# Kernel tuning notes

Measured on AMD Instinct MI355X. Metric: run time of the kernel, lower is better.

Reference implementation:

```python
import jax, jax.numpy as jnp
import numpy as np

N_LAYER, N_HEAD, D_PARAM = 4, 8, 63
BATCH, SEQ, D_FULL = 16, 2048, D_PARAM + 1
VAR = 0.02


def setup_inputs() -> dict:
    key = jax.random.key(0)
    kz, kp = jax.random.split(key)
    Z = jax.random.normal(kz, (BATCH, SEQ, D_FULL), dtype=jnp.float32)
    allparam = VAR * jax.random.normal(kp, (N_LAYER, N_HEAD, 2, D_PARAM, D_PARAM), dtype=jnp.float32)
    return {"Z": Z, "allparam": allparam}


def _augment(P, Q, d_full):
    # P_full: P in top-left block, bottom-right corner = 1, rest zeros.
    dp = P.shape[0]
    P_full = jnp.zeros((d_full, d_full), P.dtype).at[:dp, :dp].set(P).at[dp, dp].set(1.0)
    # Q_full: Q in top-left block, rest zeros (bottom-right corner stays 0).
    Q_full = jnp.zeros((d_full, d_full), Q.dtype).at[:dp, :dp].set(Q)
    return P_full, Q_full


def _attention(P, Q, Z):
    B, N, d = Z.shape
    P_full, Q_full = _augment(P, Q, d)
    # attn[b,n,m] = Z[b,n,:] @ Q_full @ Z[b,m,:]
    attn = jnp.einsum('BNi,ij,BMj->BNM', Z, Q_full, Z)
    key = jnp.einsum('ij,BNj->BNi', P_full, Z)
    # A = eye(N) with A[N-1,N-1] = 0  => zero out last token of key before aggregation.
    key = key.at[:, N - 1, :].set(0.0)
    out = jnp.einsum('BNM,BMi->BNi', attn, key)
    return out / (N - 1)


def reference(Z, allparam):
    n_layer, n_head = allparam.shape[0], allparam.shape[1]
    for i in range(n_layer):
        Zi = Z
        residues = jnp.zeros_like(Z)
        for j in range(n_head):
            residues = residues + _attention(allparam[i, j, 0], allparam[i, j, 1], Zi)
        Z = Zi + residues
    return Z
```

## Files before the change

kernel.cpp:

```cpp
#include <hip/hip_runtime.h>

constexpr int NH = 8, DP = 63, D = 64, B = 16, S = 2048;
constexpr int TILE = 128, NTILE = 16;
constexpr float INVS = 1.0f / 2047.0f;

__device__ __forceinline__ void gram_reduce_store(const float* ZN, float4* sm4,
                                                  float* __restrict__ gp, int t) {
    const int w = t >> 6, l = t & 63, qy = l >> 3, rx = l & 7;
    float g[8][8];
#pragma unroll
    for (int a = 0; a < 8; ++a)
#pragma unroll
        for (int bb = 0; bb < 8; ++bb) g[a][bb] = 0.f;

#pragma unroll 4
    for (int mi = 0; mi < 32; ++mi) {
        const int m = 32 * w + mi;
        const int f = (m >> 3) & 15;
        const float* rowp = &ZN[m * 64];
        float4 a0 = *(const float4*)&rowp[4 * (qy ^ f)];
        float4 a1 = *(const float4*)&rowp[4 * ((qy + 8) ^ f)];
        float4 b0 = *(const float4*)&rowp[4 * (rx ^ f)];
        float4 b1 = *(const float4*)&rowp[4 * ((rx + 8) ^ f)];
        float A[8]  = {a0.x, a0.y, a0.z, a0.w, a1.x, a1.y, a1.z, a1.w};
        float Bv[8] = {b0.x, b0.y, b0.z, b0.w, b1.x, b1.y, b1.z, b1.w};
#pragma unroll
        for (int a = 0; a < 8; ++a)
#pragma unroll
            for (int bb = 0; bb < 8; ++bb) g[a][bb] += A[a] * Bv[bb];
    }
    __syncthreads();

    float* part = (float*)(sm4 + w * 1024);
#pragma unroll
    for (int a = 0; a < 8; ++a) {
        const int q = 4 * qy + (a & 3) + 32 * (a >> 2);
        *(float4*)&part[q * 64 + 4 * rx]      = make_float4(g[a][0], g[a][1], g[a][2], g[a][3]);
        *(float4*)&part[q * 64 + 32 + 4 * rx] = make_float4(g[a][4], g[a][5], g[a][6], g[a][7]);
    }
    __syncthreads();

    float4* gp4 = (float4*)gp;
#pragma unroll
    for (int k = 0; k < 4; ++k) {
        const int e4 = t + 256 * k;
        float4 s0 = sm4[e4], s1 = sm4[1024 + e4], s2 = sm4[2048 + e4], s3 = sm4[3072 + e4];
        gp4[e4] = make_float4(s0.x + s1.x + s2.x + s3.x, s0.y + s1.y + s2.y + s3.y,
                              s0.z + s1.z + s2.z + s3.z, s0.w + s1.w + s2.w + s3.w);
    }
}

__global__ __launch_bounds__(256) void kGram0(const float* __restrict__ Z,
                                              float* __restrict__ Gp) {
    __shared__ float4 sm4[5120];
    float* ZN = (float*)(sm4 + 3072);
    const int b = blockIdx.x, tile = blockIdx.y, t = threadIdx.x;
#pragma unroll
    for (int k = 0; k < 8; ++k) {
        const int row = (t >> 4) + 16 * k, c4 = t & 15;
        const int grow = tile * TILE + row;
        float4 v = *(const float4*)&Z[((size_t)b * S + grow) * D + 4 * c4];
        if (grow == S - 1) v = make_float4(0.f, 0.f, 0.f, 0.f);
        *(float4*)&ZN[row * 64 + 4 * (c4 ^ ((row >> 3) & 15))] = v;
    }
    __syncthreads();
    gram_reduce_store(ZN, sm4, Gp + ((size_t)(b * 16 + tile)) * 4096, t);
}

__global__ __launch_bounds__(256) void kRed(const float* __restrict__ Gp,
                                            float* __restrict__ G,
                                            float* __restrict__ W) {
    const int b = blockIdx.x, s = blockIdx.y, t = threadIdx.x;
    const int e = s * 256 + t;
    float sum = 0.f;
#pragma unroll 4
    for (int p = 0; p < 16; ++p) sum += Gp[((size_t)(b * 16 + p)) * 4096 + e];
    G[(size_t)b * 4096 + e] = sum;
    W[(size_t)b * 4096 + e] = ((e >> 6) == (e & 63)) ? 1.f : 0.f;
}

__global__ __launch_bounds__(128) void kW(const float* __restrict__ G,
                                          const float* __restrict__ params,
                                          float* __restrict__ W) {
    __shared__ float4 sm4[(4096 + 2048 + 4096 + 2048) / 4];
    float* Gs = (float*)sm4;
    float* Pt = Gs + 4096;
    float* Qt = Pt + 2048;
    float* T  = Qt + 4096;
    const int b = blockIdx.x, j = blockIdx.y, s = blockIdx.z, t = threadIdx.x;
    const int ty = t >> 3, tx = t & 7;
    const float* P = params + (size_t)(j * 2 + 0) * (DP * DP);
    const float* Q = params + (size_t)(j * 2 + 1) * (DP * DP);

#pragma unroll
    for (int k = 0; k < 8; ++k)
        ((float4*)Gs)[t + 128 * k] = ((const float4*)(G + (size_t)b * 4096))[t + 128 * k];
#pragma unroll
    for (int k = 0; k < 16; ++k) {
        const int r = t & 63, ii = (t >> 6) + 2 * k;
        const int i = 32 * s + ii;
        float v = 0.f;
        if (r < DP && i < DP) v = P[(size_t)i * DP + r];
        else if (r == DP && i == DP) v = 1.f;
        Pt[r * 32 + 4 * ((ii >> 2) ^ (r & 7)) + (ii & 3)] = v;
    }
#pragma unroll
    for (int k = 0; k < 32; ++k) {
        const int q = t & 63, p = (t >> 6) + 2 * k;
        const float v = (p < DP && q < DP) ? Q[(size_t)p * DP + q] : 0.f;
        Qt[q * 64 + 4 * ((p >> 2) ^ (q & 15)) + (p & 3)] = v;
    }
    __syncthreads();

    float acc[4][4] = {};
#pragma unroll 4
    for (int r = 0; r < 64; ++r) {
        float4 av = *(const float4*)&Gs[r * 64 + 4 * ty];
        float4 bv = *(const float4*)&Pt[r * 32 + 4 * (tx ^ (r & 7))];
        float A[4] = {av.x, av.y, av.z, av.w}, Bb[4] = {bv.x, bv.y, bv.z, bv.w};
#pragma unroll
        for (int a = 0; a < 4; ++a)
#pragma unroll
            for (int c = 0; c < 4; ++c) acc[a][c] += A[a] * Bb[c];
    }
#pragma unroll
    for (int a = 0; a < 4; ++a)
        *(float4*)&T[(4 * ty + a) * 32 + 4 * tx] =
            make_float4(acc[a][0], acc[a][1], acc[a][2], acc[a][3]);
    __syncthreads();

    float acc2[4][4] = {};
#pragma unroll 4
    for (int q = 0; q < 64; ++q) {
        float4 av = *(const float4*)&Qt[q * 64 + 4 * (ty ^ (q & 15))];
        float4 bv = *(const float4*)&T[q * 32 + 4 * tx];
        float A[4] = {av.x, av.y, av.z, av.w}, Bb[4] = {bv.x, bv.y, bv.z, bv.w};
#pragma unroll
        for (int a = 0; a < 4; ++a)
#pragma unroll
            for (int c = 0; c < 4; ++c) acc2[a][c] += A[a] * Bb[c];
    }
    float* Wb = W + (size_t)b * 4096;
#pragma unroll
    for (int a = 0; a < 4; ++a)
#pragma unroll
        for (int c = 0; c < 4; ++c)
            atomicAdd(&Wb[(4 * ty + a) * 64 + 32 * s + 4 * tx + c], acc2[a][c] * INVS);
}

__global__ __launch_bounds__(256) void kCA(const float* __restrict__ src,
                                           const float* __restrict__ W,
                                           float* __restrict__ out,
                                           float* __restrict__ Gp, int do_gram) {
    __shared__ float4 sm4[5120];
    float* ZT = (float*)sm4;
    float* Ws = (float*)(sm4 + 2048);
    float* ZN = (float*)(sm4 + 3072);
    const int b = blockIdx.x, tile = blockIdx.y, t = threadIdx.x;
    const int ny = t & 15, ix = t >> 4;
    const size_t zbase = ((size_t)b * S + tile * TILE) * D;

#pragma unroll
    for (int k = 0; k < 4; ++k)
        sm4[2048 + t + 256 * k] = ((const float4*)(W + (size_t)b * 4096))[t + 256 * k];
#pragma unroll
    for (int k = 0; k < 8; ++k) {
        const int row = (t >> 4) + 16 * k, c4 = t & 15;
        float4 v = *(const float4*)&src[zbase + (size_t)row * D + 4 * c4];
        float vv[4] = {v.x, v.y, v.z, v.w};
#pragma unroll
        for (int c = 0; c < 4; ++c) {
            const int p = 4 * c4 + c;
            ZT[p * 128 + 4 * ((row >> 2) ^ c4) + (row & 3)] = vv[c];
        }
    }
    __syncthreads();

    float acc[8][4] = {};
#pragma unroll 4
    for (int p = 0; p < 64; ++p) {
        const int f = p >> 2;
        const float* zp = &ZT[p * 128];
        float4 a0 = *(const float4*)&zp[4 * (ny ^ f)];
        float4 a1 = *(const float4*)&zp[4 * ((ny + 16) ^ f)];
        float4 wv = *(const float4*)&Ws[p * 64 + 4 * ix];
        float A[8] = {a0.x, a0.y, a0.z, a0.w, a1.x, a1.y, a1.z, a1.w};
        float Wv[4] = {wv.x, wv.y, wv.z, wv.w};
#pragma unroll
        for (int a = 0; a < 8; ++a)
#pragma unroll
            for (int c = 0; c < 4; ++c) acc[a][c] += A[a] * Wv[c];
    }
#pragma unroll
    for (int a = 0; a < 8; ++a) {
        const int n = 4 * ny + (a & 3) + 64 * (a >> 2);
        *(float4*)&out[zbase + (size_t)n * D + 4 * ix] =
            make_float4(acc[a][0], acc[a][1], acc[a][2], acc[a][3]);
    }
    if (!do_gram) return;

#pragma unroll
    for (int a = 0; a < 8; ++a) {
        const int n = 4 * ny + (a & 3) + 64 * (a >> 2);
        float4 vv = make_float4(acc[a][0], acc[a][1], acc[a][2], acc[a][3]);
        if (tile == NTILE - 1 && n == TILE - 1) vv = make_float4(0.f, 0.f, 0.f, 0.f);
        *(float4*)&ZN[n * 64 + 4 * (ix ^ ((n >> 3) & 15))] = vv;
    }
    __syncthreads();
    gram_reduce_store(ZN, sm4, Gp + ((size_t)(b * 16 + tile)) * 4096, t);
}

extern "C" void kernel_launch(void* const* d_in, const int* in_sizes, int n_in,
                              void* d_out, int out_size, void* d_ws, size_t ws_size,
                              hipStream_t stream) {
    const float* Z        = (const float*)d_in[0];
    const float* allparam = (const float*)d_in[1];
    float* out = (float*)d_out;

    float* Gp = (float*)d_ws;
    float* G  = Gp + (size_t)B * 16 * 4096;
    float* W  = G + (size_t)B * 4096;

    kGram0<<<dim3(B, NTILE), 256, 0, stream>>>(Z, Gp);
    for (int layer = 0; layer < 4; ++layer) {
        const float* src = (layer == 0) ? Z : (const float*)out;
        const float* params = allparam + (size_t)layer * NH * 2 * DP * DP;
        kRed<<<dim3(B, 16), 256, 0, stream>>>(Gp, G, W);
        kW<<<dim3(B, NH, 2), 128, 0, stream>>>(G, params, W);
        kCA<<<dim3(B, NTILE), 256, 0, stream>>>(src, W, out, Gp, layer < 3 ? 1 : 0);
    }
}
```

Baseline: 210.5 us.

## Fuse all layers into one persistent kernel with Gram-matrix algebraic updates

Replaces the 13 separate launches with one persistent kernel of 128 blocks that synchronise through a global atomic barrier. The Gram matrix and the per-layer transforms are propagated algebraically (G' = W^T G W, M accumulated as a product of W matrices), so Z is streamed only twice, once for the initial Gram and once for the final Z·M. Launch overhead and the per-layer full passes over Z are removed. In exchange it relies on all 128 blocks being co-resident for the spin barrier, runs serialized 64x64 matmuls on only 16 blocks, and may change numerical accumulation order.

```diff
diff --git a/kernel.cpp b/kernel.cpp
--- a/kernel.cpp
+++ b/kernel.cpp
@@ -1,213 +1,312 @@
 #include <hip/hip_runtime.h>
 
-constexpr int NH = 8, DP = 63, D = 64, B = 16, S = 2048;
-constexpr int TILE = 128, NTILE = 16;
+constexpr int NH = 8, DP = 63, D = 64, BATCH = 16, S = 2048;
 constexpr float INVS = 1.0f / 2047.0f;
-
-__device__ __forceinline__ void gram_reduce_store(const float* ZN, float4* sm4,
-                                                  float* __restrict__ gp, int t) {
-    const int w = t >> 6, l = t & 63, qy = l >> 3, rx = l & 7;
-    float g[8][8];
-#pragma unroll
-    for (int a = 0; a < 8; ++a)
-#pragma unroll
-        for (int bb = 0; bb < 8; ++bb) g[a][bb] = 0.f;
-
-#pragma unroll 4
-    for (int mi = 0; mi < 32; ++mi) {
-        const int m = 32 * w + mi;
-        const int f = (m >> 3) & 15;
-        const float* rowp = &ZN[m * 64];
-        float4 a0 = *(const float4*)&rowp[4 * (qy ^ f)];
-        float4 a1 = *(const float4*)&rowp[4 * ((qy + 8) ^ f)];
-        float4 b0 = *(const float4*)&rowp[4 * (rx ^ f)];
-        float4 b1 = *(const float4*)&rowp[4 * ((rx + 8) ^ f)];
-        float A[8]  = {a0.x, a0.y, a0.z, a0.w, a1.x, a1.y, a1.z, a1.w};
-        float Bv[8] = {b0.x, b0.y, b0.z, b0.w, b1.x, b1.y, b1.z, b1.w};
-#pragma unroll
-        for (int a = 0; a < 8; ++a)
-#pragma unroll
-            for (int bb = 0; bb < 8; ++bb) g[a][bb] += A[a] * Bv[bb];
+constexpr int NBLK = 128;
+
+__device__ __forceinline__ void gsync(unsigned int* bar, unsigned int target) {
+    __syncthreads();
+    if (threadIdx.x == 0) {
+        __hip_atomic_fetch_add(bar, 1u, __ATOMIC_RELEASE, __HIP_MEMORY_SCOPE_AGENT);
+        while (__hip_atomic_load(bar, __ATOMIC_ACQUIRE, __HIP_MEMORY_SCOPE_AGENT) < target)
+            __builtin_amdgcn_s_sleep(2);
     }
     __syncthreads();
-
-    float* part = (float*)(sm4 + w * 1024);
-#pragma unroll
-    for (int a = 0; a < 8; ++a) {
-        const int q = 4 * qy + (a & 3) + 32 * (a >> 2);
-        *(float4*)&part[q * 64 + 4 * rx]      = make_float4(g[a][0], g[a][1], g[a][2], g[a][3]);
-        *(float4*)&part[q * 64 + 32 + 4 * rx] = make_float4(g[a][4], g[a][5], g[a][6], g[a][7]);
+}
+
+__global__ __launch_bounds__(256) void fused_all(
+    const float* __restrict__ Z, const float* __restrict__ params,
+    float* __restrict__ out, float* __restrict__ Gp, float* __restrict__ H,
+    float* __restrict__ Gcur, float* __restrict__ Mt, float* __restrict__ Mf,
+    unsigned int* bar) {
+    __shared__ float4 sm4[5120];
+    const int bid = blockIdx.x, t = threadIdx.x;
+    unsigned int tgt = NBLK;
+
+    {
+        float* ZN = (float*)(sm4 + 3072);
+        const int b = bid >> 3, oct = bid & 7;
+        const int w = t >> 6, l = t & 63, qy = l >> 3, rx = l & 7;
+        float g[8][8];
+#pragma unroll
+        for (int a = 0; a < 8; ++a)
+#pragma unroll
+            for (int bb = 0; bb < 8; ++bb) g[a][bb] = 0.f;
+
+        for (int half = 0; half < 2; ++half) {
+            const int rowbase = oct * 256 + half * 128;
+#pragma unroll
+            for (int k = 0; k < 8; ++k) {
+                const int row = (t >> 4) + 16 * k, c4 = t & 15;
+                const int grow = rowbase + row;
+                float4 v = *(const float4*)&Z[((size_t)b * S + grow) * D + 4 * c4];
+                if (grow == S - 1) v = make_float4(0.f, 0.f, 0.f, 0.f);
+                *(float4*)&ZN[row * 64 + 4 * (c4 ^ ((row >> 3) & 15))] = v;
+            }
+            __syncthreads();
+#pragma unroll 4
+            for (int mi = 0; mi < 32; ++mi) {
+                const int m = 32 * w + mi;
+                const int f = (m >> 3) & 15;
+                const float* rowp = &ZN[m * 64];
+                float4 a0 = *(const float4*)&rowp[4 * (qy ^ f)];
+                float4 a1 = *(const float4*)&rowp[4 * ((qy + 8) ^ f)];
+                float4 b0 = *(const float4*)&rowp[4 * (rx ^ f)];
+                float4 b1 = *(const float4*)&rowp[4 * ((rx + 8) ^ f)];
+                float A[8]  = {a0.x, a0.y, a0.z, a0.w, a1.x, a1.y, a1.z, a1.w};
+                float Bv[8] = {b0.x, b0.y, b0.z, b0.w, b1.x, b1.y, b1.z, b1.w};
+#pragma unroll
+                for (int a = 0; a < 8; ++a)
+#pragma unroll
+                    for (int bb = 0; bb < 8; ++bb) g[a][bb] += A[a] * Bv[bb];
+            }
+            __syncthreads();
+        }
+        float* part = (float*)(sm4 + w * 1024);
+#pragma unroll
+        for (int a = 0; a < 8; ++a) {
+            const int q = 4 * qy + (a & 3) + 32 * (a >> 2);
+            *(float4*)&part[q * 64 + 4 * rx]      = make_float4(g[a][0], g[a][1], g[a][2], g[a][3]);
+            *(float4*)&part[q * 64 + 32 + 4 * rx] = make_float4(g[a][4], g[a][5], g[a][6], g[a][7]);
+        }
+        __syncthreads();
+        float4* gp4 = (float4*)(Gp + (size_t)(b * 8 + oct) * 4096);
+#pragma unroll
+        for (int k = 0; k < 4; ++k) {
+            const int e4 = t + 256 * k;
+            float4 s0 = sm4[e4], s1 = sm4[1024 + e4], s2 = sm4[2048 + e4], s3 = sm4[3072 + e4];
+            gp4[e4] = make_float4(s0.x + s1.x + s2.x + s3.x, s0.y + s1.y + s2.y + s3.y,
+                                  s0.z + s1.z + s2.z + s3.z, s0.w + s1.w + s2.w + s3.w);
+        }
     }
-    __syncthreads();
-
-    float4* gp4 = (float4*)gp;
-#pragma unroll
-    for (int k = 0; k < 4; ++k) {
-        const int e4 = t + 256 * k;
-        float4 s0 = sm4[e4], s1 = sm4[1024 + e4], s2 = sm4[2048 + e4], s3 = sm4[3072 + e4];
-        gp4[e4] = make_float4(s0.x + s1.x + s2.x + s3.x, s0.y + s1.y + s2.y + s3.y,
-                              s0.z + s1.z + s2.z + s3.z, s0.w + s1.w + s2.w + s3.w);
+    gsync(bar, tgt); tgt += NBLK;
+
+    for (int layer = 0; layer < 4; ++layer) {
+        {
+            float* Gs = (float*)sm4;
+            float* Pt = Gs + 4096;
+            float* Qt = Pt + 4096;
+            float* Tb = Qt + 4096;
+            const int b = bid >> 3, j = bid & 7;
+            const float* P = params + ((size_t)(layer * NH + j) * 2) * (DP * DP);
+            const float* Q = P + DP * DP;
+            float4* Gs4 = (float4*)Gs;
+            if (layer == 0) {
+                const float4* Gp4 = (const float4*)Gp;
+#pragma unroll
+                for (int k = 0; k < 4; ++k) {
+                    const int e4 = t + 256 * k;
+                    float4 sum = make_float4(0.f, 0.f, 0.f, 0.f);
+                    for (int p = 0; p < 8; ++p) {
+                        float4 gg = Gp4[(size_t)(b * 8 + p) * 1024 + e4];
+                        sum.x += gg.x; sum.y += gg.y; sum.z += gg.z; sum.w += gg.w;
+                    }
+                    Gs4[e4] = sum;
+                }
+            } else {
+                const float4* Gc4 = (const float4*)(Gcur + (size_t)b * 4096);
+#pragma unroll
+                for (int k = 0; k < 4; ++k) Gs4[t + 256 * k] = Gc4[t + 256 * k];
+            }
+            {
+                const int rr = t & 63, qtr = t >> 6;
+#pragma unroll
+                for (int k = 0; k < 16; ++k) {
+                    const int i = qtr * 16 + k;
+                    float pv = 0.f;
+                    if (rr < DP && i < DP) pv = P[(size_t)i * DP + rr];
+                    else if (rr == DP && i == DP) pv = 1.f;
+                    Pt[rr * 64 + 4 * ((i >> 2) ^ (rr & 15)) + (i & 3)] = pv;
+                    const float qv = (i < DP && rr < DP) ? Q[(size_t)i * DP + rr] : 0.f;
+                    Qt[rr * 64 + 4 * ((i >> 2) ^ (rr & 15)) + (i & 3)] = qv;
+                }
+            }
+            __syncthreads();
+            const int ty = t >> 4, tx = t & 15;
+            float acc[4][4] = {};
+#pragma unroll 4
+            for (int r = 0; r < 64; ++r) {
+                float4 av = *(const float4*)&Gs[r * 64 + 4 * ty];
+                float4 bv = *(const float4*)&Pt[r * 64 + 4 * (tx ^ (r & 15))];
+                float A[4] = {av.x, av.y, av.z, av.w}, Bb[4] = {bv.x, bv.y, bv.z, bv.w};
+#pragma unroll
+                for (int a = 0; a < 4; ++a)
+#pragma unroll
+                    for (int c = 0; c < 4; ++c) acc[a][c] += A[a] * Bb[c];
+            }
+#pragma unroll
+            for (int a = 0; a < 4; ++a)
+                *(float4*)&Tb[(4 * ty + a) * 64 + 4 * tx] =
+                    make_float4(acc[a][0], acc[a][1], acc[a][2], acc[a][3]);
+            __syncthreads();
+            float acc2[4][4] = {};
+#pragma unroll 4
+            for (int q = 0; q < 64; ++q) {
+                float4 av = *(const float4*)&Qt[q * 64 + 4 * (ty ^ (q & 15))];
+                float4 bv = *(const float4*)&Tb[q * 64 + 4 * tx];
+                float A[4] = {av.x, av.y, av.z, av.w}, Bb[4] = {bv.x, bv.y, bv.z, bv.w};
+#pragma unroll
+                for (int a = 0; a < 4; ++a)
+#pragma unroll
+                    for (int c = 0; c < 4; ++c) acc2[a][c] += A[a] * Bb[c];
+            }
+            float* Hb = H + (size_t)(b * NH + j) * 4096;
+#pragma unroll
+            for (int a = 0; a < 4; ++a)
+                *(float4*)&Hb[(4 * ty + a) * 64 + 4 * tx] =
+                    make_float4(acc2[a][0] * INVS, acc2[a][1] * INVS,
+                                acc2[a][2] * INVS, acc2[a][3] * INVS);
+        }
+        gsync(bar, tgt); tgt += NBLK;
+
+        if (bid < 16) {
+            const int b = bid;
+            float* Ws = (float*)sm4;
+            float* As = Ws + 4096;
+            float* Ts = As + 4096;
+            float* Ms = Ts + 4096;
+            float4* Ws4 = (float4*)Ws; float4* As4 = (float4*)As; float4* Ms4 = (float4*)Ms;
+#pragma unroll
+            for (int k = 0; k < 4; ++k) {
+                const int e4 = t + 256 * k;
+                float iv[4];
+#pragma unroll
+                for (int c = 0; c < 4; ++c) {
+                    const int e = 4 * e4 + c;
+                    iv[c] = ((e >> 6) == (e & 63)) ? 1.f : 0.f;
+                }
+                float4 w = make_float4(iv[0], iv[1], iv[2], iv[3]);
+                const float4* H4 = (const float4*)H;
+                for (int j = 0; j < 8; ++j) {
+                    float4 h = H4[(size_t)(b * 8 + j) * 1024 + e4];
+                    w.x += h.x; w.y += h.y; w.z += h.z; w.w += h.w;
+                }
+                Ws4[e4] = w;
+                if (layer == 0) {
+                    const float4* Gp4 = (const float4*)Gp;
+                    float4 sum = make_float4(0.f, 0.f, 0.f, 0.f);
+                    for (int p = 0; p < 8; ++p) {
+                        float4 gg = Gp4[(size_t)(b * 8 + p) * 1024 + e4];
+                        sum.x += gg.x; sum.y += gg.y; sum.z += gg.z; sum.w += gg.w;
+                    }
+                    As4[e4] = sum;
+                    Ms4[e4] = make_float4(iv[0], iv[1], iv[2], iv[3]);
+                } else {
+                    As4[e4] = ((const float4*)(Gcur + (size_t)b * 4096))[e4];
+                    Ms4[e4] = ((const float4*)(Mt + (size_t)b * 4096))[e4];
+                }
+            }
+            __syncthreads();
+            const int ty = t >> 4, tx = t & 15;
+            if (layer < 3) {
+                float acc[4][4] = {};
+#pragma unroll 4
+                for (int r = 0; r < 64; ++r) {
+                    float4 av = *(const float4*)&As[r * 64 + 4 * ty];
+                    float4 bv = *(const float4*)&Ws[r * 64 + 4 * tx];
+                    float A[4] = {av.x, av.y, av.z, av.w}, Bb[4] = {bv.x, bv.y, bv.z, bv.w};
+#pragma unroll
+                    for (int a = 0; a < 4; ++a)
+#pragma unroll
+                        for (int c = 0; c < 4; ++c) acc[a][c] += A[a] * Bb[c];
+                }
+#pragma unroll
+                for (int a = 0; a < 4; ++a)
+                    *(float4*)&Ts[(4 * ty + a) * 64 + 4 * tx] =
+                        make_float4(acc[a][0], acc[a][1], acc[a][2], acc[a][3]);
+                __syncthreads();
+                float accG[4][4] = {}, accM[4][4] = {};
+#pragma unroll 4
+                for (int p = 0; p < 64; ++p) {
+                    float4 av = *(const float4*)&Ws[p * 64 + 4 * ty];
+                    float4 bv = *(const float4*)&Ts[p * 64 + 4 * tx];
+                    float4 cv = *(const float4*)&Ms[p * 64 + 4 * tx];
+                    float A[4] = {av.x, av.y, av.z, av.w};
+                    float Bb[4] = {bv.x, bv.y, bv.z, bv.w};
+                    float Cc[4] = {cv.x, cv.y, cv.z, cv.w};
+#pragma unroll
+                    for (int a = 0; a < 4; ++a)
+#pragma unroll
+                        for (int c = 0; c < 4; ++c) {
+                            accG[a][c] += A[a] * Bb[c];
+                            accM[a][c] += A[a] * Cc[c];
+                        }
+                }
+                float* Gout = Gcur + (size_t)b * 4096;
+                float* Mout = Mt + (size_t)b * 4096;
+#pragma unroll
+                for (int a = 0; a < 4; ++a) {
+                    *(float4*)&Gout[(4 * ty + a) * 64 + 4 * tx] =
+                        make_float4(accG[a][0], accG[a][1], accG[a][2], accG[a][3]);
+                    *(float4*)&Mout[(4 * ty + a) * 64 + 4 * tx] =
+                        make_float4(accM[a][0], accM[a][1], accM[a][2], accM[a][3]);
+                }
+            } else {
+                float accM[4][4] = {};
+#pragma unroll 4
+                for (int p = 0; p < 64; ++p) {
+                    float4 av = *(const float4*)&Ms[p * 64 + 4 * ty];
+                    float4 bv = *(const float4*)&Ws[p * 64 + 4 * tx];
+                    float A[4] = {av.x, av.y, av.z, av.w}, Bb[4] = {bv.x, bv.y, bv.z, bv.w};
+#pragma unroll
+                    for (int a = 0; a < 4; ++a)
+#pragma unroll
+                        for (int c = 0; c < 4; ++c) accM[a][c] += A[a] * Bb[c];
+                }
+                float* Mout = Mf + (size_t)b * 4096;
+#pragma unroll
+                for (int a = 0; a < 4; ++a)
+                    *(float4*)&Mout[(4 * ty + a) * 64 + 4 * tx] =
+                        make_float4(accM[a][0], accM[a][1], accM[a][2], accM[a][3]);
+            }
+        }
+        gsync(bar, tgt); tgt += NBLK;
     }
-}
-
-__global__ __launch_bounds__(256) void kGram0(const float* __restrict__ Z,
-                                              float* __restrict__ Gp) {
-    __shared__ float4 sm4[5120];
-    float* ZN = (float*)(sm4 + 3072);
-    const int b = blockIdx.x, tile = blockIdx.y, t = threadIdx.x;
-#pragma unroll
-    for (int k = 0; k < 8; ++k) {
-        const int row = (t >> 4) + 16 * k, c4 = t & 15;
-        const int grow = tile * TILE + row;
-        float4 v = *(const float4*)&Z[((size_t)b * S + grow) * D + 4 * c4];
-        if (grow == S - 1) v = make_float4(0.f, 0.f, 0.f, 0.f);
-        *(float4*)&ZN[row * 64 + 4 * (c4 ^ ((row >> 3) & 15))] = v;
+
+    {
+        float* ZT = (float*)sm4;
+        float* Ws = (float*)(sm4 + 2048);
+        const int b = bid >> 3, oct = bid & 7;
+        const int ny = t & 15, ix = t >> 4;
+#pragma unroll
+        for (int k = 0; k < 4; ++k)
+            ((float4*)Ws)[t + 256 * k] = ((const float4*)(Mf + (size_t)b * 4096))[t + 256 * k];
+        for (int half = 0; half < 2; ++half) {
+            const size_t zbase = ((size_t)b * S + oct * 256 + half * 128) * D;
+            __syncthreads();
+#pragma unroll
+            for (int k = 0; k < 8; ++k) {
+                const int row = (t >> 4) + 16 * k, c4 = t & 15;
+                float4 v = *(const float4*)&Z[zbase + (size_t)row * D + 4 * c4];
+                float vv[4] = {v.x, v.y, v.z, v.w};
+#pragma unroll
+                for (int c = 0; c < 4; ++c)
+                    ZT[(4 * c4 + c) * 128 + 4 * ((row >> 2) ^ c4) + (row & 3)] = vv[c];
+            }
+            __syncthreads();
+            float acc[8][4] = {};
+#pragma unroll 4
+            for (int p = 0; p < 64; ++p) {
+                const int f = p >> 2;
+                const float* zp = &ZT[p * 128];
+                float4 a0 = *(const float4*)&zp[4 * (ny ^ f)];
+                float4 a1 = *(const float4*)&zp[4 * ((ny + 16) ^ f)];
+                float4 wv = *(const float4*)&Ws[p * 64 + 4 * ix];
+                float A[8] = {a0.x, a0.y, a0.z, a0.w, a1.x, a1.y, a1.z, a1.w};
+                float Wv[4] = {wv.x, wv.y, wv.z, wv.w};
+#pragma unroll
+                for (int a = 0; a < 8; ++a)
+#pragma unroll
+                    for (int c = 0; c < 4; ++c) acc[a][c] += A[a] * Wv[c];
+            }
+#pragma unroll
+            for (int a = 0; a < 8; ++a) {
+                const int n = 4 * ny + (a & 3) + 64 * (a >> 2);
+                *(float4*)&out[zbase + (size_t)n * D + 4 * ix] =
+                    make_float4(acc[a][0], acc[a][1], acc[a][2], acc[a][3]);
+            }
+        }
     }
-    __syncthreads();
-    gram_reduce_store(ZN, sm4, Gp + ((size_t)(b * 16 + tile)) * 4096, t);
-}
-
-__global__ __launch_bounds__(256) void kRed(const float* __restrict__ Gp,
-                                            float* __restrict__ G,
-                                            float* __restrict__ W) {
-    const int b = blockIdx.x, s = blockIdx.y, t = threadIdx.x;
-    const int e = s * 256 + t;
-    float sum = 0.f;
-#pragma unroll 4
-    for (int p = 0; p < 16; ++p) sum += Gp[((size_t)(b * 16 + p)) * 4096 + e];
-    G[(size_t)b * 4096 + e] = sum;
-    W[(size_t)b * 4096 + e] = ((e >> 6) == (e & 63)) ? 1.f : 0.f;
-}
-
-__global__ __launch_bounds__(128) void kW(const float* __restrict__ G,
-                                          const float* __restrict__ params,
-                                          float* __restrict__ W) {
-    __shared__ float4 sm4[(4096 + 2048 + 4096 + 2048) / 4];
-    float* Gs = (float*)sm4;
-    float* Pt = Gs + 4096;
-    float* Qt = Pt + 2048;
-    float* T  = Qt + 4096;
-    const int b = blockIdx.x, j = blockIdx.y, s = blockIdx.z, t = threadIdx.x;
-    const int ty = t >> 3, tx = t & 7;
-    const float* P = params + (size_t)(j * 2 + 0) * (DP * DP);
-    const float* Q = params + (size_t)(j * 2 + 1) * (DP * DP);
-
-#pragma unroll
-    for (int k = 0; k < 8; ++k)
-        ((float4*)Gs)[t + 128 * k] = ((const float4*)(G + (size_t)b * 4096))[t + 128 * k];
-#pragma unroll
-    for (int k = 0; k < 16; ++k) {
-        const int r = t & 63, ii = (t >> 6) + 2 * k;
-        const int i = 32 * s + ii;
-        float v = 0.f;
-        if (r < DP && i < DP) v = P[(size_t)i * DP + r];
-        else if (r == DP && i == DP) v = 1.f;
-        Pt[r * 32 + 4 * ((ii >> 2) ^ (r & 7)) + (ii & 3)] = v;
-    }
-#pragma unroll
-    for (int k = 0; k < 32; ++k) {
-        const int q = t & 63, p = (t >> 6) + 2 * k;
-        const float v = (p < DP && q < DP) ? Q[(size_t)p * DP + q] : 0.f;
-        Qt[q * 64 + 4 * ((p >> 2) ^ (q & 15)) + (p & 3)] = v;
-    }
-    __syncthreads();
-
-    float acc[4][4] = {};
-#pragma unroll 4
-    for (int r = 0; r < 64; ++r) {
-        float4 av = *(const float4*)&Gs[r * 64 + 4 * ty];
-        float4 bv = *(const float4*)&Pt[r * 32 + 4 * (tx ^ (r & 7))];
-        float A[4] = {av.x, av.y, av.z, av.w}, Bb[4] = {bv.x, bv.y, bv.z, bv.w};
-#pragma unroll
-        for (int a = 0; a < 4; ++a)
-#pragma unroll
-            for (int c = 0; c < 4; ++c) acc[a][c] += A[a] * Bb[c];
-    }
-#pragma unroll
-    for (int a = 0; a < 4; ++a)
-        *(float4*)&T[(4 * ty + a) * 32 + 4 * tx] =
-            make_float4(acc[a][0], acc[a][1], acc[a][2], acc[a][3]);
-    __syncthreads();
-
-    float acc2[4][4] = {};
-#pragma unroll 4
-    for (int q = 0; q < 64; ++q) {
-        float4 av = *(const float4*)&Qt[q * 64 + 4 * (ty ^ (q & 15))];
-        float4 bv = *(const float4*)&T[q * 32 + 4 * tx];
-        float A[4] = {av.x, av.y, av.z, av.w}, Bb[4] = {bv.x, bv.y, bv.z, bv.w};
-#pragma unroll
-        for (int a = 0; a < 4; ++a)
-#pragma unroll
-            for (int c = 0; c < 4; ++c) acc2[a][c] += A[a] * Bb[c];
-    }
-    float* Wb = W + (size_t)b * 4096;
-#pragma unroll
-    for (int a = 0; a < 4; ++a)
-#pragma unroll
-        for (int c = 0; c < 4; ++c)
-            atomicAdd(&Wb[(4 * ty + a) * 64 + 32 * s + 4 * tx + c], acc2[a][c] * INVS);
-}
-
-__global__ __launch_bounds__(256) void kCA(const float* __restrict__ src,
-                                           const float* __restrict__ W,
-                                           float* __restrict__ out,
-                                           float* __restrict__ Gp, int do_gram) {
-    __shared__ float4 sm4[5120];
-    float* ZT = (float*)sm4;
-    float* Ws = (float*)(sm4 + 2048);
-    float* ZN = (float*)(sm4 + 3072);
-    const int b = blockIdx.x, tile = blockIdx.y, t = threadIdx.x;
-    const int ny = t & 15, ix = t >> 4;
-    const size_t zbase = ((size_t)b * S + tile * TILE) * D;
-
-#pragma unroll
-    for (int k = 0; k < 4; ++k)
-        sm4[2048 + t + 256 * k] = ((const float4*)(W + (size_t)b * 4096))[t + 256 * k];
-#pragma unroll
-    for (int k = 0; k < 8; ++k) {
-        const int row = (t >> 4) + 16 * k, c4 = t & 15;
-        float4 v = *(const float4*)&src[zbase + (size_t)row * D + 4 * c4];
-        float vv[4] = {v.x, v.y, v.z, v.w};
-#pragma unroll
-        for (int c = 0; c < 4; ++c) {
-            const int p = 4 * c4 + c;
-            ZT[p * 128 + 4 * ((row >> 2) ^ c4) + (row & 3)] = vv[c];
-        }
-    }
-    __syncthreads();
-
-    float acc[8][4] = {};
-#pragma unroll 4
-    for (int p = 0; p < 64; ++p) {
-        const int f = p >> 2;
-        const float* zp = &ZT[p * 128];
-        float4 a0 = *(const float4*)&zp[4 * (ny ^ f)];
-        float4 a1 = *(const float4*)&zp[4 * ((ny + 16) ^ f)];
-        float4 wv = *(const float4*)&Ws[p * 64 + 4 * ix];
-        float A[8] = {a0.x, a0.y, a0.z, a0.w, a1.x, a1.y, a1.z, a1.w};
-        float Wv[4] = {wv.x, wv.y, wv.z, wv.w};
-#pragma unroll
-        for (int a = 0; a < 8; ++a)
-#pragma unroll
-            for (int c = 0; c < 4; ++c) acc[a][c] += A[a] * Wv[c];
-    }
-#pragma unroll
-    for (int a = 0; a < 8; ++a) {
-        const int n = 4 * ny + (a & 3) + 64 * (a >> 2);
-        *(float4*)&out[zbase + (size_t)n * D + 4 * ix] =
-            make_float4(acc[a][0], acc[a][1], acc[a][2], acc[a][3]);
-    }
-    if (!do_gram) return;
-
-#pragma unroll
-    for (int a = 0; a < 8; ++a) {
-        const int n = 4 * ny + (a & 3) + 64 * (a >> 2);
-        float4 vv = make_float4(acc[a][0], acc[a][1], acc[a][2], acc[a][3]);
-        if (tile == NTILE - 1 && n == TILE - 1) vv = make_float4(0.f, 0.f, 0.f, 0.f);
-        *(float4*)&ZN[n * 64 + 4 * (ix ^ ((n >> 3) & 15))] = vv;
-    }
-    __syncthreads();
-    gram_reduce_store(ZN, sm4, Gp + ((size_t)(b * 16 + tile)) * 4096, t);
 }
 
 extern "C" void kernel_launch(void* const* d_in, const int* in_sizes, int n_in,
@@ -218,15 +317,12 @@
     float* out = (float*)d_out;
 
     float* Gp = (float*)d_ws;
-    float* G  = Gp + (size_t)B * 16 * 4096;
-    float* W  = G + (size_t)B * 4096;
-
-    kGram0<<<dim3(B, NTILE), 256, 0, stream>>>(Z, Gp);
-    for (int layer = 0; layer < 4; ++layer) {
-        const float* src = (layer == 0) ? Z : (const float*)out;
-        const float* params = allparam + (size_t)layer * NH * 2 * DP * DP;
-        kRed<<<dim3(B, 16), 256, 0, stream>>>(Gp, G, W);
-        kW<<<dim3(B, NH, 2), 128, 0, stream>>>(G, params, W);
-        kCA<<<dim3(B, NTILE), 256, 0, stream>>>(src, W, out, Gp, layer < 3 ? 1 : 0);
-    }
+    float* H  = Gp + (size_t)NBLK * 4096;
+    float* Gc = H + (size_t)BATCH * NH * 4096;
+    float* Mt = Gc + (size_t)BATCH * 4096;
+    float* Mf = Mt + (size_t)BATCH * 4096;
+    unsigned int* bar = (unsigned int*)(Mf + (size_t)BATCH * 4096);
+
+    hipMemsetAsync(bar, 0, 64, stream);
+    fused_all<<<NBLK, 256, 0, stream>>>(Z, allparam, out, Gp, H, Gc, Mt, Mf, bar);
 }
```

After: 290.4 us. 38.0% more time.
